# Kernel tuning notes

Hardware: AMD Instinct MI355X
Metric: run time of the kernel (lower is better)

Reference implementation:

```python
import jax, jax.numpy as jnp
import numpy as np
from jax import lax

RATE = 2
KSIZE = 3
STRIDE = 1
FUSE_K = 3
SCALE = 10.0
DN = ('NCHW', 'OIHW', 'NCHW')


def extract_patches(x, k, s):
    # x: [B,C,H,W] -> [B,nH,nW,C,k,k]  (ZeroPad2d(1) when k != 1, as in torch code)
    B, C, H, W = x.shape
    p = 0 if k == 1 else 1
    xp = jnp.pad(x, ((0, 0), (0, 0), (p, p), (p, p)))
    nH = (H + 2 * p - k) // s + 1
    nW = (W + 2 * p - k) // s + 1
    cols = [xp[:, :, di:di + s * nH:s, dj:dj + s * nW:s]
            for di in range(k) for dj in range(k)]
    pat = jnp.stack(cols, 0).reshape(k, k, B, C, nH, nW)
    return pat.transpose(2, 4, 5, 3, 0, 1)


def _fuse(y):
    # conv of the [L,L] score image with eye(FUSE_K) kernel, same padding
    # == sum of diagonal shifts of the zero-padded image
    L = y.shape[0]
    p = (FUSE_K - 1) // 2
    A = jnp.pad(y, ((p, p), (p, p)))
    out = A[0:L, 0:L]
    for d in range(1, FUSE_K):
        out = out + A[d:d + L, d:d + L]
    return out


def _per_sample(xi, wi, raw_wi, mmi, h, w):
    # xi: [C,h,w]  wi: [L,C,3,3]  raw_wi: [L,C,4,4]  mmi: [L,1,1]
    L = h * w
    norm = jnp.sqrt(jnp.sum(wi * wi, axis=(1, 2, 3), keepdims=True))
    wi_n = wi / jnp.maximum(norm, 1e-4)
    # cosine-similarity conv: [L,h,w]
    yi = lax.conv_general_dilated(xi[None], wi_n, (1, 1), ((1, 1), (1, 1)),
                                  dimension_numbers=DN)[0]
    # fuse pass 1 on [L(patch), L(spatial)]
    y = _fuse(yi.reshape(L, L))
    # transpose (h_p,w_p,h',w') -> (w_p,h_p,w',h'), fuse pass 2, transpose back
    y = y.reshape(h, w, h, w).transpose(1, 0, 3, 2).reshape(L, L)
    y = _fuse(y)
    y = y.reshape(w, h, w, h).transpose(1, 0, 3, 2).reshape(L, h, w)
    y = y * mmi
    y = jax.nn.softmax(y * SCALE, axis=0)
    y = jnp.maximum(y * mmi, 1e-8)
    # conv_transpose2d(y, raw_wi, stride=2, padding=1) as lhs-dilated conv
    Wf = raw_wi[:, :, ::-1, ::-1].transpose(1, 0, 2, 3)  # [C,L,4,4]
    out = lax.conv_general_dilated(y[None], Wf, (1, 1), ((2, 2), (2, 2)),
                                   lhs_dilation=(2, 2),
                                   dimension_numbers=DN)[0]
    return out / 4.0


def reference(x1, x2, mask):
    B, C, H, W = x1.shape
    kernel = 2 * RATE
    raw_w = extract_patches(x1, kernel, RATE * STRIDE)
    x2s = x2[:, :, ::2, ::2]          # F.interpolate scale=0.5, nearest
    h, w = x2s.shape[2], x2s.shape[3]
    L = h * w
    raw_w = raw_w.reshape(B, L, C, kernel, kernel)
    wpat = extract_patches(x2s, KSIZE, STRIDE).reshape(B, L, C, KSIZE, KSIZE)
    # mask is already [B,1,h,w]: bilinear align_corners resize to (h,w) is identity
    m = extract_patches(mask, KSIZE, STRIDE).reshape(B, L, -1).mean(axis=2)
    mm = (m == 0.0).astype(x1.dtype)[:, :, None, None]  # [B,L,1,1]
    f = lambda xi, wi, rwi, mmi: _per_sample(xi, wi, rwi, mmi, h, w)
    return jax.vmap(f)(x2s, wpat, raw_w, mm)  # [B,C,H,W]


def setup_inputs() -> dict:
    key = jax.random.key(0)
    k1, k2 = jax.random.split(key)
    x1 = jax.random.normal(k1, (2, 128, 96, 96), dtype=jnp.float32)
    x2 = jax.random.normal(k2, (2, 128, 96, 96), dtype=jnp.float32)
    mask = jnp.zeros((2, 1, 48, 48), dtype=jnp.float32)
    return {"x1": x1, "x2": x2, "mask": mask}
```

## Files before the change

### kernel.cpp

```cpp
#include <hip/hip_runtime.h>
#include <hip/hip_bf16.h>

#define Cc   128
#define Hh   96
#define hs   48
#define Ls   2304
#define CK   2048
#define KG   384

typedef __attribute__((ext_vector_type(8))) short short8;
typedef __attribute__((ext_vector_type(4))) float f32x4;

__device__ __forceinline__ unsigned short f2bf(float x) {
    unsigned int u = __float_as_uint(x);
    unsigned int r = (u + 0x7fff + ((u >> 16) & 1)) >> 16;
    return (unsigned short)r;
}
__device__ __forceinline__ float bf2f(unsigned short h) {
    return __uint_as_float((unsigned)h << 16);
}

__device__ __forceinline__ f32x4 ld4u(const float* p) {
    f32x4 v; __builtin_memcpy(&v, p, 16); return v;
}

#define GLOAD_LDS16(g, l) \
    __builtin_amdgcn_global_load_lds((__attribute__((address_space(1))) const void*)(g), \
                                     (__attribute__((address_space(3))) void*)(l), 16, 0, 0)


__global__ __launch_bounds__(256) void transposePQ_k(const float* __restrict__ x2,
                                                     unsigned short* __restrict__ P,
                                                     unsigned short* __restrict__ Q,
                                                     long long sPQ, int z0) {
    const int z = z0 + blockIdx.z;
    const float* x2b = x2 + (size_t)z * Cc * Hh * Hh;
    unsigned short* Pb = P + (size_t)blockIdx.z * sPQ;
    unsigned short* Qb = Q + (size_t)blockIdx.z * sPQ;
    __shared__ float tile[64][65];
    const int c0 = blockIdx.x * 64;
    const int l0 = blockIdx.y * 64;
    const int t = threadIdx.x;
    const int lt = t & 63, cg = t >> 6;
    const int l = l0 + lt;
    const int iy = l / hs, jx = l % hs;
    const int srcoff = iy * (2 * Hh) + 2 * jx;
#pragma unroll
    for (int cc = 0; cc < 16; ++cc) {
        int c = cg * 16 + cc;
        tile[lt][c] = x2b[(size_t)(c0 + c) * (Hh * Hh) + srcoff];
    }
    __syncthreads();
    const int lr = t >> 2, seg = t & 3;
    const int lw = l0 + lr;
    short8 hv0, hv1, lv0, lv1;
#pragma unroll
    for (int k = 0; k < 8; ++k) {
        float x = tile[lr][seg * 16 + k];
        unsigned short h = f2bf(x);
        float hf = __uint_as_float((unsigned)h << 16);
        unsigned short lo = f2bf(x - hf);
        hv0[k] = (short)h; lv0[k] = (short)lo;
    }
#pragma unroll
    for (int k = 0; k < 8; ++k) {
        float x = tile[lr][seg * 16 + 8 + k];
        unsigned short h = f2bf(x);
        float hf = __uint_as_float((unsigned)h << 16);
        unsigned short lo = f2bf(x - hf);
        hv1[k] = (short)h; lv1[k] = (short)lo;
    }
    size_t rowp = (size_t)lw * KG;
    int coff = c0 + seg * 16;
    *(short8*)&Pb[rowp + coff] = hv0;        *(short8*)&Pb[rowp + coff + 8] = hv1;
    *(short8*)&Pb[rowp + 128 + coff] = lv0;  *(short8*)&Pb[rowp + 128 + coff + 8] = lv1;
    *(short8*)&Pb[rowp + 256 + coff] = hv0;  *(short8*)&Pb[rowp + 256 + coff + 8] = hv1;
    *(short8*)&Qb[rowp + coff] = hv0;        *(short8*)&Qb[rowp + coff + 8] = hv1;
    *(short8*)&Qb[rowp + 128 + coff] = hv0;  *(short8*)&Qb[rowp + 128 + coff + 8] = hv1;
    *(short8*)&Qb[rowp + 256 + coff] = lv0;  *(short8*)&Qb[rowp + 256 + coff + 8] = lv1;
}

__global__ __launch_bounds__(256) void mm_k(const float* __restrict__ mask, float* __restrict__ MM) {
    int z = blockIdx.y;
    const float* mb = mask + (size_t)z * hs * hs;
    float* MMb = MM + (size_t)z * Ls;
    int l = blockIdx.x * 256 + threadIdx.x;
    if (l >= Ls) return;
    int ly = l / hs, lx = l % hs;
    float s = 0.f;
    for (int dy = -1; dy <= 1; ++dy)
        for (int dx = -1; dx <= 1; ++dx) {
            int yy = ly + dy, xx = lx + dx;
            if ((unsigned)yy < (unsigned)hs && (unsigned)xx < (unsigned)hs) s += mb[yy * hs + xx];
        }
    float m = s * (1.0f / 9.0f);
    MMb[l] = (m == 0.0f) ? 1.0f : 0.0f;
}

__global__ __launch_bounds__(256) void taps9rn_k(const float* __restrict__ G, float* __restrict__ S,
                                                 float* __restrict__ RN, long long zsG, long long zsS, int z0) {
    const float* Gb = G + (size_t)blockIdx.z * zsG;
    float* Sb = S + (size_t)blockIdx.z * zsS;
    float* RNb = RN + (size_t)(z0 + blockIdx.z) * Ls;
    int g = blockIdx.x * 256 + threadIdx.x;
    int i = g / 576;
    int jb = (g - i * 576) * 4;
    int iy = i / hs, ix = i % hs;
    int jy = jb / hs, jx0 = jb % hs;
    f32x4 acc = {};
#pragma unroll
    for (int dy = -1; dy <= 1; ++dy) {
        int vy = ((unsigned)(iy + dy) < (unsigned)hs) && ((unsigned)(jy + dy) < (unsigned)hs);
#pragma unroll
        for (int dx = -1; dx <= 1; ++dx) {
            int vi = vy && ((unsigned)(ix + dx) < (unsigned)hs);
            int o = hs * dy + dx;
            int row = vi ? (i + o) : i;
            f32x4 v = ld4u(&Gb[(size_t)row * Ls + jb + o]);
            f32x4 m;
#pragma unroll
            for (int ln = 0; ln < 4; ++ln)
                m[ln] = (vi && ((unsigned)(jx0 + ln + dx) < (unsigned)hs)) ? 1.f : 0.f;
            acc += v * m;
        }
    }
    __builtin_memcpy(&Sb[(size_t)i * Ls + jb], &acc, 16);
    int dd = i - jb;
    if ((unsigned)dd < 4u) RNb[i] = 1.0f / fmaxf(sqrtf(acc[dd]), 1e-4f);
}

__global__ __launch_bounds__(256) void fuse12T_k(const float* __restrict__ S, const float* __restrict__ RN,
                                                 float* __restrict__ ZT, long long zsS, long long zsZT, int z0) {
    const float* Sb = S + (size_t)blockIdx.z * zsS;
    float* ZTb = ZT + (size_t)blockIdx.z * zsZT;
    const float* RNb = RN + (size_t)(z0 + blockIdx.z) * Ls;
    __shared__ float tile[64][65];
    const int i0 = blockIdx.y * 64, j0 = blockIdx.x * 64;
    const int t = threadIdx.x;
    const int jg = t & 15, tit = t >> 4;
    const int jb = j0 + jg * 4;
    const int jy0 = jb / hs, jx0 = jb % hs;

    int ccb[9]; f32x4 m4[9];
#pragma unroll
    for (int d2 = -1; d2 <= 1; ++d2) {
        int cl[4], vb[4];
#pragma unroll
        for (int ln = 0; ln < 4; ++ln) {
            int j2 = (jx0 + ln) * hs + jy0 + d2;
            int vv = ((unsigned)j2 < (unsigned)Ls) ? 1 : 0;
            int c = vv ? ((j2 % hs) * hs + j2 / hs) : 0;
            cl[ln] = c; vb[ln] = vv;
        }
        int base = 0;
#pragma unroll
        for (int ln = 0; ln < 4; ++ln) if (vb[ln]) base = cl[ln] - ln;
#pragma unroll
        for (int d1 = -1; d1 <= 1; ++d1) {
            int idx = (d2 + 1) * 3 + (d1 + 1);
            ccb[idx] = base + d1;
            f32x4 mm;
#pragma unroll
            for (int ln = 0; ln < 4; ++ln) {
                int cc = cl[ln] + d1;
                mm[ln] = (vb[ln] && ((unsigned)cc < (unsigned)Ls)) ? 1.f : 0.f;
            }
            m4[idx] = mm;
        }
    }

    f32x4 acc[4] = {};
#pragma unroll
    for (int kk = 0; kk < 4; ++kk) {
        const int i = i0 + tit * 4 + kk;
        const int iy = i / hs, ix = i % hs;
        const int tif = ix * hs + iy;
#pragma unroll
        for (int d2 = -1; d2 <= 1; ++d2) {
            int i2 = tif + d2;
            int vi = ((unsigned)i2 < (unsigned)Ls) ? 1 : 0;
            int r = vi ? ((i2 % hs) * hs + i2 / hs) : 1;
#pragma unroll
            for (int d1 = -1; d1 <= 1; ++d1) {
                int rr = r + d1;
                int vr = vi && ((unsigned)rr < (unsigned)Ls);
                int rrc = vr ? rr : 0;
                float w = RNb[rrc];
                w = vr ? w : 0.f;
                int idx = (d2 + 1) * 3 + (d1 + 1);
                f32x4 v = ld4u(&Sb[(size_t)rrc * Ls + ccb[idx]]);
                acc[kk] += v * m4[idx] * w;
            }
        }
    }
#pragma unroll
    for (int kk = 0; kk < 4; ++kk) {
        int ti = tit * 4 + kk;
        tile[ti][jg * 4 + 0] = acc[kk][0];
        tile[ti][jg * 4 + 1] = acc[kk][1];
        tile[ti][jg * 4 + 2] = acc[kk][2];
        tile[ti][jg * 4 + 3] = acc[kk][3];
    }
    __syncthreads();
    const int r2 = t >> 2, cs = (t & 3) * 16;
    float vbuf[16];
#pragma unroll
    for (int k = 0; k < 16; ++k) vbuf[k] = tile[cs + k][r2];
    float* dst = &ZTb[(size_t)(j0 + r2) * Ls + i0 + cs];
#pragma unroll
    for (int k = 0; k < 4; ++k)
        *(float4*)&dst[k * 4] = *(float4*)&vbuf[k * 4];
}

__global__ __launch_bounds__(256) void softmax_row_k(const float* __restrict__ ZT, const float* __restrict__ MM,
                                                     unsigned short* __restrict__ AT, long long zsZT, int z0) {
    const int z = z0 + blockIdx.z;
    const float* ZTb = ZT + (size_t)blockIdx.z * zsZT;
    const float* MMb = MM + (size_t)z * Ls;
    unsigned short* ATb = AT + (size_t)z * Ls * Ls;
    const int w = threadIdx.x >> 6, lane = threadIdx.x & 63;
    const int p = blockIdx.x * 4 + w;
    const float* row = ZTb + (size_t)p * Ls;
    float v[36];
    float mx = -3.4e38f;
#pragma unroll
    for (int k = 0; k < 9; ++k) {
        const float4 zv = *(const float4*)&row[k * 256 + lane * 4];
        const float4 m = *(const float4*)&MMb[k * 256 + lane * 4];
        v[4 * k + 0] = zv.x * m.x * 10.f;
        v[4 * k + 1] = zv.y * m.y * 10.f;
        v[4 * k + 2] = zv.z * m.z * 10.f;
        v[4 * k + 3] = zv.w * m.w * 10.f;
        mx = fmaxf(mx, fmaxf(fmaxf(v[4 * k], v[4 * k + 1]), fmaxf(v[4 * k + 2], v[4 * k + 3])));
    }
#pragma unroll
    for (int off = 32; off; off >>= 1) mx = fmaxf(mx, __shfl_xor(mx, off));
    float sum = 0.f;
#pragma unroll
    for (int kk = 0; kk < 36; ++kk) { v[kk] = __expf(v[kk] - mx); sum += v[kk]; }
#pragma unroll
    for (int off = 32; off; off >>= 1) sum += __shfl_xor(sum, off);
    const float rs = 1.0f / sum;
#pragma unroll
    for (int k = 0; k < 9; ++k) {
        const float4 m = *(const float4*)&MMb[k * 256 + lane * 4];
        ushort4 o;
        o.x = f2bf(fmaxf(v[4 * k + 0] * rs * m.x, 1e-8f));
        o.y = f2bf(fmaxf(v[4 * k + 1] * rs * m.y, 1e-8f));
        o.z = f2bf(fmaxf(v[4 * k + 2] * rs * m.z, 1e-8f));
        o.w = f2bf(fmaxf(v[4 * k + 3] * rs * m.w, 1e-8f));
        *(ushort4*)&ATb[(size_t)p * Ls + k * 256 + lane * 4] = o;
    }
}

__global__ __launch_bounds__(256) void gather_rwT_k(const float* __restrict__ x1, unsigned short* __restrict__ RWT) {
    const int z = blockIdx.z;
    const float* x1b = x1 + (size_t)z * Cc * Hh * Hh;
    unsigned short* R = RWT + (size_t)z * CK * Ls;
    int idx = blockIdx.x * 256 + threadIdx.x;
    int ck = idx / 288;
    int lg = idx - ck * 288;
    int l0 = lg * 8;
    int ly = lg / 6;
    int lx0 = (lg - ly * 6) * 8;
    int c = ck >> 4, a = (ck >> 2) & 3, b2 = ck & 3;
    int u = 2 * ly + a - 1;
    short8 o = {};
    if ((unsigned)u < (unsigned)Hh) {
        const float* row = x1b + (size_t)c * (Hh * Hh) + (size_t)u * Hh;
#pragma unroll
        for (int e = 0; e < 8; ++e) {
            int vv = 2 * (lx0 + e) + b2 - 1;
            o[e] = (short)(((unsigned)vv < (unsigned)Hh) ? f2bf(row[vv]) : (unsigned short)0);
        }
    }
    *(short8*)&R[(size_t)ck * Ls + l0] = o;
}

__global__ __launch_bounds__(256) void scatter3_k(const unsigned short* __restrict__ T, float* __restrict__ out) {
    const int z = blockIdx.z;
    const int c = blockIdx.x;
    const int yh = blockIdx.y;
    const unsigned short* Tb = T + (size_t)z * Ls * CK + (size_t)c * 16;
    float* outb = out + (size_t)z * Cc * Hh * Hh + (size_t)c * Hh * Hh;
    const int i0 = (yh == 0) ? 0 : 23;
    __shared__ unsigned short Tl[1200 * 16];
    const int t = threadIdx.x;
#pragma unroll
    for (int rep = 0; rep < 5; ++rep) {
        int p = rep * 256 + t;
        if (p < 1200)
            __builtin_memcpy(&Tl[p * 16], &Tb[(size_t)(i0 * hs + p) * CK], 32);
    }
    __syncthreads();
#pragma unroll
    for (int rep = 0; rep < 5; ++rep) {
        int idx4 = rep * 256 + t;
        if (idx4 >= 1152) break;
        int Y = yh * 48 + idx4 / 24;
        int X0 = (idx4 % 24) * 4;
        float o4[4];
#pragma unroll
        for (int xi = 0; xi < 4; ++xi) {
            int X = X0 + xi;
            int a0 = (Y + 1) & 1, b0 = (X + 1) & 1;
            float s = 0.f;
#pragma unroll
            for (int ai = 0; ai < 2; ++ai) {
                int a = a0 + 2 * ai;
                int i = (Y + 1 - a) >> 1;
                if ((unsigned)i >= (unsigned)hs) continue;
#pragma unroll
                for (int bi = 0; bi < 2; ++bi) {
                    int b2 = b0 + 2 * bi;
                    int jj = (X + 1 - b2) >> 1;
                    if ((unsigned)jj >= (unsigned)hs) continue;
                    s += bf2f(Tl[((i - i0) * hs + jj) * 16 + a * 4 + b2]);
                }
            }
            o4[xi] = 0.25f * s;
        }
        *(float4*)&outb[Y * Hh + X0] = *(float4*)&o4[0];
    }
}

template <int SUPER, int CBF16>
__global__ __launch_bounds__(256) void mfma_gemm_k(const unsigned short* __restrict__ A,
                                                   const unsigned short* __restrict__ Bt,
                                                   void* __restrict__ Cv, int M, int N, int K,
                                                   long long sA, long long sB, long long sC) {
    A  += (size_t)blockIdx.z * sA;
    Bt += (size_t)blockIdx.z * sB;
    float* Cf = (float*)Cv + (CBF16 ? 0 : (size_t)blockIdx.z * sC);
    unsigned short* Ch = (unsigned short*)Cv + (CBF16 ? (size_t)blockIdx.z * sC : 0);

    const int nb = gridDim.x * gridDim.y;
    const int flat = blockIdx.y * gridDim.x + blockIdx.x;
    const int q = nb >> 3, r = nb & 7;
    const int xcd = flat & 7, sidx = flat >> 3;
    const int wg = (xcd < r ? xcd * (q + 1) : r * (q + 1) + (xcd - r) * q) + sidx;
    int bm, bn;
    if (SUPER) {
        int st = wg / 12, tt = wg % 12;
        int stn = st & 3, stm = st >> 2;
        int tn = tt & 3, tm = tt >> 2;
        bn = (stn * 4 + tn) * 128;
        bm = (stm * 3 + tm) * 128;
    } else {
        bm = (wg / gridDim.x) * 128;
        bn = (wg % gridDim.x) * 128;
    }

    __shared__ __align__(16) unsigned short Asm[3][128 * 32];
    __shared__ __align__(16) unsigned short Bsm[3][128 * 32];
    const int t = threadIdx.x;
    const int lane = t & 63, w = t >> 6;
    const int wr = w >> 1, wc = w & 1;

    const int rA = 32 * w + (lane >> 2);
    const int kA = (((lane & 3) ^ ((lane >> 3) & 3))) * 8;
    const unsigned short* gA0 = A + (size_t)(bm + rA) * K + kA;
    const unsigned short* gA1 = gA0 + (size_t)16 * K;
    const unsigned short* gB0 = Bt + (size_t)(bn + rA) * K + kA;
    const unsigned short* gB1 = gB0 + (size_t)16 * K;

#define STAGE4(b, koff) do { \
        GLOAD_LDS16(gA0 + (koff), &Asm[b][(2 * w) * 512]); \
        GLOAD_LDS16(gA1 + (koff), &Asm[b][(2 * w + 1) * 512]); \
        GLOAD_LDS16(gB0 + (koff), &Bsm[b][(2 * w) * 512]); \
        GLOAD_LDS16(gB1 + (koff), &Bsm[b][(2 * w + 1) * 512]); \
    } while (0)

    const int fr = lane & 15, fq = lane >> 4;
    const int sqa = (fq ^ ((fr >> 1) & 3)) * 8;
    f32x4 acc[4][4] = {};

    const int nt = K >> 5;
    STAGE4(0, 0);
    STAGE4(1, 32);
    asm volatile("s_waitcnt vmcnt(4)" ::: "memory");
    __builtin_amdgcn_s_barrier();
    __builtin_amdgcn_sched_barrier(0);

    int cur = 0;
    for (int tt = 0; tt < nt; ++tt) {
        if (tt + 2 < nt) STAGE4((tt + 2) % 3, (tt + 2) * 32);
        short8 av[4], bv[4];
#pragma unroll
        for (int m = 0; m < 4; ++m)
            av[m] = *(const short8*)&Asm[cur][(wr * 64 + m * 16 + fr) * 32 + sqa];
#pragma unroll
        for (int n = 0; n < 4; ++n)
            bv[n] = *(const short8*)&Bsm[cur][(wc * 64 + n * 16 + fr) * 32 + sqa];
#pragma unroll
        for (int m = 0; m < 4; ++m)
#pragma unroll
            for (int n = 0; n < 4; ++n)
                acc[m][n] = __builtin_amdgcn_mfma_f32_16x16x32_bf16(av[m], bv[n], acc[m][n], 0, 0, 0);
        __builtin_amdgcn_sched_barrier(0);
        if (tt + 1 < nt) {
            if (tt + 2 < nt)
                asm volatile("s_waitcnt vmcnt(4)" ::: "memory");
            else
                asm volatile("s_waitcnt vmcnt(0)" ::: "memory");
            __builtin_amdgcn_s_barrier();
            __builtin_amdgcn_sched_barrier(0);
        }
        cur = (cur + 1) % 3;
    }
#undef STAGE4

#pragma unroll
    for (int m = 0; m < 4; ++m) {
        int row0 = bm + wr * 64 + m * 16 + fq * 4;
#pragma unroll
        for (int n = 0; n < 4; ++n) {
            int col = bn + wc * 64 + n * 16 + fr;
#pragma unroll
            for (int rr = 0; rr < 4; ++rr) {
                if (CBF16)
                    Ch[(size_t)(row0 + rr) * N + col] = f2bf(acc[m][n][rr]);
                else
                    Cf[(size_t)(row0 + rr) * N + col] = acc[m][n][rr];
            }
        }
    }
}


extern "C" void kernel_launch(void* const* d_in, const int* in_sizes, int n_in,
                              void* d_out, int out_size, void* d_ws, size_t ws_size,
                              hipStream_t stream) {
    const float* x1 = (const float*)d_in[0];
    const float* x2 = (const float*)d_in[1];
    const float* mask = (const float*)d_in[2];
    float* out = (float*)d_out;

    char* base = (char*)d_ws;
    const size_t LsLs = (size_t)Ls * Ls;
    const size_t LsCK = (size_t)Ls * CK;
    const long long sPQ = (long long)Ls * KG;

    const bool batched = ws_size >= 132175872ull;

    float* MM2 = (float*)(base);
    float* RN2 = (float*)(base + 20480);
    unsigned short *P, *Q, *ATb2, *RWT2;
    float *G, *S;
    unsigned short* T2 = (unsigned short*)base;
    if (batched) {
        P    = (unsigned short*)(base + 40960);
        Q    = (unsigned short*)(base + 3584000);
        G    = (float*)(base + 7127040);
        S    = (float*)(base + 49598464);
        ATb2 = (unsigned short*)(base + 92067840);
        RWT2 = (unsigned short*)(base + 113301504);
    } else {
        P    = (unsigned short*)(base + 40960);
        Q    = (unsigned short*)(base + 1812480);
        G    = (float*)(base + 3586048);
        S    = (float*)(base + 24823808);
        ATb2 = (unsigned short*)(base + 46059520);
        RWT2 = (unsigned short*)(base + 67293184);
    }

    mm_k<<<dim3(Ls / 256, 2), 256, 0, stream>>>(mask, MM2);
    gather_rwT_k<<<dim3((CK * 288) / 256, 1, 2), 256, 0, stream>>>(x1, RWT2);

    const int tapsGrid = (Ls * 576) / 256;

    if (batched) {
        transposePQ_k<<<dim3(2, Ls / 64, 2), 256, 0, stream>>>(x2, P, Q, sPQ, 0);
        mfma_gemm_k<0, 0><<<dim3(Ls / 128, Ls / 128, 2), 256, 0, stream>>>(
            P, Q, G, Ls, Ls, KG, sPQ, sPQ, (long long)LsLs);
        taps9rn_k<<<dim3(tapsGrid, 1, 2), 256, 0, stream>>>(G, S, RN2, (long long)LsLs, (long long)LsLs, 0);
        fuse12T_k<<<dim3(Ls / 64, Ls / 64, 2), 256, 0, stream>>>(S, RN2, G, (long long)LsLs, (long long)LsLs, 0);
        softmax_row_k<<<dim3(Ls / 4, 1, 2), 256, 0, stream>>>(G, MM2, ATb2, (long long)LsLs, 0);
    } else {
        for (int z0 = 0; z0 < 2; ++z0) {
            transposePQ_k<<<dim3(2, Ls / 64, 1), 256, 0, stream>>>(x2, P, Q, 0, z0);
            mfma_gemm_k<0, 0><<<dim3(Ls / 128, Ls / 128, 1), 256, 0, stream>>>(
                P, Q, G, Ls, Ls, KG, 0, 0, 0);
            taps9rn_k<<<dim3(tapsGrid, 1, 1), 256, 0, stream>>>(G, S, RN2, 0, 0, z0);
            fuse12T_k<<<dim3(Ls / 64, Ls / 64, 1), 256, 0, stream>>>(S, RN2, G, 0, 0, z0);
            softmax_row_k<<<dim3(Ls / 4, 1, 1), 256, 0, stream>>>(G, MM2, ATb2, 0, z0);
        }
    }

    mfma_gemm_k<1, 1><<<dim3(CK / 128, Ls / 128, 2), 256, 0, stream>>>(
        ATb2, RWT2, T2, Ls, CK, Ls,
        (long long)LsLs, (long long)LsCK, (long long)LsCK);

    scatter3_k<<<dim3(Cc, 2, 2), 256, 0, stream>>>(T2, out);

    (void)in_sizes; (void)n_in; (void)out_size; (void)ws_size;
}
```

Baseline: 237.7 us.

## Fuse transposed-conv scatter into GEMM epilogue via atomics; use double-buffered LDS

The final GEMM now scatters its results straight into the output image using float atomicAdd with the 0.25 scale, after a memset of the output. This removes the bf16 intermediate T buffer and the separate scatter3_k kernel. The shared GEMM kernel also drops from a 3-stage LDS pipeline with explicit vmcnt waits to a simple 2-stage double buffer with __syncthreads, which affects both GEMMs. The cost is millions of global atomics, some contention since each output pixel gets several contributions, and weaker load/compute overlap in the main loops.

```diff
diff --git a/kernel.cpp b/kernel.cpp
--- a/kernel.cpp
+++ b/kernel.cpp
@@ -277,62 +277,14 @@
     *(short8*)&R[(size_t)ck * Ls + l0] = o;
 }
 
-__global__ __launch_bounds__(256) void scatter3_k(const unsigned short* __restrict__ T, float* __restrict__ out) {
-    const int z = blockIdx.z;
-    const int c = blockIdx.x;
-    const int yh = blockIdx.y;
-    const unsigned short* Tb = T + (size_t)z * Ls * CK + (size_t)c * 16;
-    float* outb = out + (size_t)z * Cc * Hh * Hh + (size_t)c * Hh * Hh;
-    const int i0 = (yh == 0) ? 0 : 23;
-    __shared__ unsigned short Tl[1200 * 16];
-    const int t = threadIdx.x;
-#pragma unroll
-    for (int rep = 0; rep < 5; ++rep) {
-        int p = rep * 256 + t;
-        if (p < 1200)
-            __builtin_memcpy(&Tl[p * 16], &Tb[(size_t)(i0 * hs + p) * CK], 32);
-    }
-    __syncthreads();
-#pragma unroll
-    for (int rep = 0; rep < 5; ++rep) {
-        int idx4 = rep * 256 + t;
-        if (idx4 >= 1152) break;
-        int Y = yh * 48 + idx4 / 24;
-        int X0 = (idx4 % 24) * 4;
-        float o4[4];
-#pragma unroll
-        for (int xi = 0; xi < 4; ++xi) {
-            int X = X0 + xi;
-            int a0 = (Y + 1) & 1, b0 = (X + 1) & 1;
-            float s = 0.f;
-#pragma unroll
-            for (int ai = 0; ai < 2; ++ai) {
-                int a = a0 + 2 * ai;
-                int i = (Y + 1 - a) >> 1;
-                if ((unsigned)i >= (unsigned)hs) continue;
-#pragma unroll
-                for (int bi = 0; bi < 2; ++bi) {
-                    int b2 = b0 + 2 * bi;
-                    int jj = (X + 1 - b2) >> 1;
-                    if ((unsigned)jj >= (unsigned)hs) continue;
-                    s += bf2f(Tl[((i - i0) * hs + jj) * 16 + a * 4 + b2]);
-                }
-            }
-            o4[xi] = 0.25f * s;
-        }
-        *(float4*)&outb[Y * Hh + X0] = *(float4*)&o4[0];
-    }
-}
-
-template <int SUPER, int CBF16>
+template <int SUPER, int MODE>
 __global__ __launch_bounds__(256) void mfma_gemm_k(const unsigned short* __restrict__ A,
                                                    const unsigned short* __restrict__ Bt,
                                                    void* __restrict__ Cv, int M, int N, int K,
                                                    long long sA, long long sB, long long sC) {
     A  += (size_t)blockIdx.z * sA;
     Bt += (size_t)blockIdx.z * sB;
-    float* Cf = (float*)Cv + (CBF16 ? 0 : (size_t)blockIdx.z * sC);
-    unsigned short* Ch = (unsigned short*)Cv + (CBF16 ? (size_t)blockIdx.z * sC : 0);
+    float* Cf = (float*)Cv + (size_t)blockIdx.z * sC;
 
     const int nb = gridDim.x * gridDim.y;
     const int flat = blockIdx.y * gridDim.x + blockIdx.x;
@@ -351,8 +303,8 @@
         bn = (wg % gridDim.x) * 128;
     }
 
-    __shared__ __align__(16) unsigned short Asm[3][128 * 32];
-    __shared__ __align__(16) unsigned short Bsm[3][128 * 32];
+    __shared__ __align__(16) unsigned short Asm[2][128 * 32];
+    __shared__ __align__(16) unsigned short Bsm[2][128 * 32];
     const int t = threadIdx.x;
     const int lane = t & 63, w = t >> 6;
     const int wr = w >> 1, wc = w & 1;
@@ -377,14 +329,10 @@
 
     const int nt = K >> 5;
     STAGE4(0, 0);
-    STAGE4(1, 32);
-    asm volatile("s_waitcnt vmcnt(4)" ::: "memory");
-    __builtin_amdgcn_s_barrier();
-    __builtin_amdgcn_sched_barrier(0);
-
+    __syncthreads();
     int cur = 0;
     for (int tt = 0; tt < nt; ++tt) {
-        if (tt + 2 < nt) STAGE4((tt + 2) % 3, (tt + 2) * 32);
+        if (tt + 1 < nt) STAGE4(cur ^ 1, (tt + 1) * 32);
         short8 av[4], bv[4];
 #pragma unroll
         for (int m = 0; m < 4; ++m)
@@ -397,31 +345,40 @@
 #pragma unroll
             for (int n = 0; n < 4; ++n)
                 acc[m][n] = __builtin_amdgcn_mfma_f32_16x16x32_bf16(av[m], bv[n], acc[m][n], 0, 0, 0);
-        __builtin_amdgcn_sched_barrier(0);
-        if (tt + 1 < nt) {
-            if (tt + 2 < nt)
-                asm volatile("s_waitcnt vmcnt(4)" ::: "memory");
-            else
-                asm volatile("s_waitcnt vmcnt(0)" ::: "memory");
-            __builtin_amdgcn_s_barrier();
-            __builtin_amdgcn_sched_barrier(0);
-        }
-        cur = (cur + 1) % 3;
+        __syncthreads();
+        cur ^= 1;
     }
 #undef STAGE4
 
-#pragma unroll
-    for (int m = 0; m < 4; ++m) {
-        int row0 = bm + wr * 64 + m * 16 + fq * 4;
-#pragma unroll
-        for (int n = 0; n < 4; ++n) {
-            int col = bn + wc * 64 + n * 16 + fr;
+    if (MODE == 0) {
+#pragma unroll
+        for (int m = 0; m < 4; ++m) {
+            int row0 = bm + wr * 64 + m * 16 + fq * 4;
+#pragma unroll
+            for (int n = 0; n < 4; ++n) {
+                int col = bn + wc * 64 + n * 16 + fr;
+#pragma unroll
+                for (int rr = 0; rr < 4; ++rr)
+                    Cf[(size_t)(row0 + rr) * N + col] = acc[m][n][rr];
+            }
+        }
+    } else {
+#pragma unroll
+        for (int m = 0; m < 4; ++m) {
+            int row0 = bm + wr * 64 + m * 16 + fq * 4;
 #pragma unroll
             for (int rr = 0; rr < 4; ++rr) {
-                if (CBF16)
-                    Ch[(size_t)(row0 + rr) * N + col] = f2bf(acc[m][n][rr]);
-                else
-                    Cf[(size_t)(row0 + rr) * N + col] = acc[m][n][rr];
+                int p = row0 + rr;
+                int i = p / hs, j = p - i * hs;
+                int Yb = 2 * i - 1, Xb = 2 * j - 1;
+#pragma unroll
+                for (int n = 0; n < 4; ++n) {
+                    int col = bn + wc * 64 + n * 16 + fr;
+                    int c = col >> 4, a = (col >> 2) & 3, b2 = col & 3;
+                    int Y = Yb + a, X = Xb + b2;
+                    if ((unsigned)Y < (unsigned)Hh && (unsigned)X < (unsigned)Hh)
+                        atomicAdd(&Cf[(size_t)c * (Hh * Hh) + Y * Hh + X], 0.25f * acc[m][n][rr]);
+                }
             }
         }
     }
@@ -447,7 +404,6 @@
     float* RN2 = (float*)(base + 20480);
     unsigned short *P, *Q, *ATb2, *RWT2;
     float *G, *S;
-    unsigned short* T2 = (unsigned short*)base;
     if (batched) {
         P    = (unsigned short*)(base + 40960);
         Q    = (unsigned short*)(base + 3584000);
@@ -463,6 +419,8 @@
         ATb2 = (unsigned short*)(base + 46059520);
         RWT2 = (unsigned short*)(base + 67293184);
     }
+
+    hipMemsetAsync(d_out, 0, (size_t)out_size * sizeof(float), stream);
 
     mm_k<<<dim3(Ls / 256, 2), 256, 0, stream>>>(mask, MM2);
     gather_rwT_k<<<dim3((CK * 288) / 256, 1, 2), 256, 0, stream>>>(x1, RWT2);
@@ -487,11 +445,9 @@
         }
     }
 
-    mfma_gemm_k<1, 1><<<dim3(CK / 128, Ls / 128, 2), 256, 0, stream>>>(
-        ATb2, RWT2, T2, Ls, CK, Ls,
-        (long long)LsLs, (long long)LsCK, (long long)LsCK);
-
-    scatter3_k<<<dim3(Cc, 2, 2), 256, 0, stream>>>(T2, out);
-
-    (void)in_sizes; (void)n_in; (void)out_size; (void)ws_size;
-}
+    mfma_gemm_k<1, 2><<<dim3(CK / 128, Ls / 128, 2), 256, 0, stream>>>(
+        ATb2, RWT2, out, Ls, CK, Ls,
+        (long long)LsLs, (long long)LsCK, (long long)(Cc * Hh * Hh));
+
+    (void)in_sizes; (void)n_in; (void)ws_size;
+}
```

New measurement: 277.5 us. 16.7% more time.

## Double-buffer GEMM LDS staging and widen taps kernel to eight columns

Applied to the files above, without the earlier changes.

The bf16 MFMA GEMM drops from a three-stage LDS ring with hand-placed vmcnt waits and raw barriers to a two-stage ping-pong. Each stage is now guarded by a plain __syncthreads, which cuts LDS use and simplifies synchronisation. The cost is that each prefetch has only one iteration to land, so less memory latency is hidden. Separately, the 9-tap fuse kernel has each thread produce eight output columns instead of four, halving the grid and amortising index and mask arithmetic.

```diff
diff --git a/kernel.cpp b/kernel.cpp
--- a/kernel.cpp
+++ b/kernel.cpp
@@ -103,11 +103,11 @@
     float* Sb = S + (size_t)blockIdx.z * zsS;
     float* RNb = RN + (size_t)(z0 + blockIdx.z) * Ls;
     int g = blockIdx.x * 256 + threadIdx.x;
-    int i = g / 576;
-    int jb = (g - i * 576) * 4;
+    int i = g / 288;
+    int jb = (g - i * 288) * 8;
     int iy = i / hs, ix = i % hs;
     int jy = jb / hs, jx0 = jb % hs;
-    f32x4 acc = {};
+    f32x4 acc0 = {}, acc1 = {};
 #pragma unroll
     for (int dy = -1; dy <= 1; ++dy) {
         int vy = ((unsigned)(iy + dy) < (unsigned)hs) && ((unsigned)(jy + dy) < (unsigned)hs);
@@ -116,17 +116,32 @@
             int vi = vy && ((unsigned)(ix + dx) < (unsigned)hs);
             int o = hs * dy + dx;
             int row = vi ? (i + o) : i;
-            f32x4 v = ld4u(&Gb[(size_t)row * Ls + jb + o]);
-            f32x4 m;
-#pragma unroll
-            for (int ln = 0; ln < 4; ++ln)
-                m[ln] = (vi && ((unsigned)(jx0 + ln + dx) < (unsigned)hs)) ? 1.f : 0.f;
-            acc += v * m;
-        }
-    }
-    __builtin_memcpy(&Sb[(size_t)i * Ls + jb], &acc, 16);
-    int dd = i - jb;
-    if ((unsigned)dd < 4u) RNb[i] = 1.0f / fmaxf(sqrtf(acc[dd]), 1e-4f);
+            const float* src = &Gb[(size_t)row * Ls + jb + o];
+            f32x4 v0 = ld4u(src);
+            f32x4 v1 = ld4u(src + 4);
+            f32x4 m0, m1;
+#pragma unroll
+            for (int ln = 0; ln < 4; ++ln) {
+                m0[ln] = (vi && ((unsigned)(jx0 + ln + dx) < (unsigned)hs)) ? 1.f : 0.f;
+                m1[ln] = (vi && ((unsigned)(jx0 + 4 + ln + dx) < (unsigned)hs)) ? 1.f : 0.f;
+            }
+            acc0 += v0 * m0;
+            acc1 += v1 * m1;
+        }
+    }
+    float* dst = &Sb[(size_t)i * Ls + jb];
+    __builtin_memcpy(dst, &acc0, 16);
+    __builtin_memcpy(dst + 4, &acc1, 16);
+    unsigned dd = (unsigned)(i - jb);
+    if (dd < 8u) {
+        float dv = 0.f;
+#pragma unroll
+        for (int e = 0; e < 4; ++e) {
+            if (dd == (unsigned)e) dv = acc0[e];
+            if (dd == (unsigned)(e + 4)) dv = acc1[e];
+        }
+        RNb[i] = 1.0f / fmaxf(sqrtf(dv), 1e-4f);
+    }
 }
 
 __global__ __launch_bounds__(256) void fuse12T_k(const float* __restrict__ S, const float* __restrict__ RN,
@@ -351,8 +366,8 @@
         bn = (wg % gridDim.x) * 128;
     }
 
-    __shared__ __align__(16) unsigned short Asm[3][128 * 32];
-    __shared__ __align__(16) unsigned short Bsm[3][128 * 32];
+    __shared__ __align__(16) unsigned short Asm[2][128 * 32];
+    __shared__ __align__(16) unsigned short Bsm[2][128 * 32];
     const int t = threadIdx.x;
     const int lane = t & 63, w = t >> 6;
     const int wr = w >> 1, wc = w & 1;
@@ -377,14 +392,10 @@
 
     const int nt = K >> 5;
     STAGE4(0, 0);
-    STAGE4(1, 32);
-    asm volatile("s_waitcnt vmcnt(4)" ::: "memory");
-    __builtin_amdgcn_s_barrier();
-    __builtin_amdgcn_sched_barrier(0);
-
+    __syncthreads();
     int cur = 0;
     for (int tt = 0; tt < nt; ++tt) {
-        if (tt + 2 < nt) STAGE4((tt + 2) % 3, (tt + 2) * 32);
+        if (tt + 1 < nt) STAGE4(cur ^ 1, (tt + 1) * 32);
         short8 av[4], bv[4];
 #pragma unroll
         for (int m = 0; m < 4; ++m)
@@ -397,16 +408,8 @@
 #pragma unroll
             for (int n = 0; n < 4; ++n)
                 acc[m][n] = __builtin_amdgcn_mfma_f32_16x16x32_bf16(av[m], bv[n], acc[m][n], 0, 0, 0);
-        __builtin_amdgcn_sched_barrier(0);
-        if (tt + 1 < nt) {
-            if (tt + 2 < nt)
-                asm volatile("s_waitcnt vmcnt(4)" ::: "memory");
-            else
-                asm volatile("s_waitcnt vmcnt(0)" ::: "memory");
-            __builtin_amdgcn_s_barrier();
-            __builtin_amdgcn_sched_barrier(0);
-        }
-        cur = (cur + 1) % 3;
+        __syncthreads();
+        cur ^= 1;
     }
 #undef STAGE4
 
@@ -467,7 +470,7 @@
     mm_k<<<dim3(Ls / 256, 2), 256, 0, stream>>>(mask, MM2);
     gather_rwT_k<<<dim3((CK * 288) / 256, 1, 2), 256, 0, stream>>>(x1, RWT2);
 
-    const int tapsGrid = (Ls * 576) / 256;
+    const int tapsGrid = (Ls * 288) / 256;
 
     if (batched) {
         transposePQ_k<<<dim3(2, Ls / 64, 2), 256, 0, stream>>>(x2, P, Q, sPQ, 0);
```

Result: slower. 244.3 us (+2.7%).
